# Performance work log

Hardware: AMD Instinct MI355X
Metric: run time of the kernel (lower is better)

Reference implementation:

```python
import jax, jax.numpy as jnp
import numpy as np

T, B, I, H = 512, 64, 1024, 1024
DROPOUT = 0.3


def setup_inputs() -> dict:
    key = jax.random.key(0)
    k = jax.random.split(key, 6)
    s = 1.0 / np.sqrt(H).astype(np.float32)
    x = jax.random.normal(k[0], (T, B, I), dtype=jnp.float32)
    w_ih = jax.random.uniform(k[1], (4 * H, I), minval=-s, maxval=s, dtype=jnp.float32)
    w_hh = jax.random.uniform(k[2], (4 * H, H), minval=-s, maxval=s, dtype=jnp.float32)
    b_ih = jax.random.uniform(k[3], (4 * H,), minval=-s, maxval=s, dtype=jnp.float32)
    b_hh = jax.random.uniform(k[4], (4 * H,), minval=-s, maxval=s, dtype=jnp.float32)
    # init_weights: forget-gate bias (second quarter) set to 1
    b_ih = b_ih.at[H:2 * H].set(1.0)
    b_hh = b_hh.at[H:2 * H].set(1.0)
    # DropConnect mask on recurrent weights (training-mode dropout, fixed realization)
    keep = jax.random.bernoulli(k[5], 1.0 - DROPOUT, (4 * H, H))
    hh_mask = keep.astype(jnp.float32) / (1.0 - DROPOUT)
    return {"x": x, "w_ih": w_ih, "w_hh": w_hh, "b_ih": b_ih, "b_hh": b_hh, "hh_mask": hh_mask}


def reference(x, w_ih, w_hh, b_ih, b_hh, hh_mask):
    # x: (T, B, I). PyTorch LSTM gate order: i, f, g, o.
    h = w_hh.shape[1]
    w_hh_dropped = w_hh * hh_mask  # DropConnect applied once per forward
    # Precompute input contribution for all timesteps (one big GEMM): (T, B, 4H)
    gx = jnp.einsum('tbi,gi->tbg', x, w_ih) + b_ih + b_hh

    def step(carry, g_t):
        h_t, c_t = carry
        gates = g_t + h_t @ w_hh_dropped.T  # (B, 4H)
        i_g, f_g, g_g, o_g = jnp.split(gates, 4, axis=-1)
        i_g = jax.nn.sigmoid(i_g)
        f_g = jax.nn.sigmoid(f_g)
        g_g = jnp.tanh(g_g)
        o_g = jax.nn.sigmoid(o_g)
        c_new = f_g * c_t + i_g * g_g
        h_new = o_g * jnp.tanh(c_new)
        return (h_new, c_new), h_new

    bsz = x.shape[1]
    init = (jnp.zeros((bsz, h), x.dtype), jnp.zeros((bsz, h), x.dtype))
    (hn, cn), out = jax.lax.scan(step, init, gx)
    # match torch: output (T,B,H), hn/cn with leading num_layers dim
    return out, hn[None], cn[None]
```

## Files before the change

### kernel.cpp

```cpp
#include <hip/hip_runtime.h>

#define TT 512
#define BB 64
#define II 1024
#define HH 1024
#define GG 4096
#define BH 65536
#define NBLK 128

typedef __attribute__((ext_vector_type(8))) short bf16x8;
typedef __attribute__((ext_vector_type(4))) float f32x4;
typedef __attribute__((ext_vector_type(4))) unsigned u32x4;

__device__ __forceinline__ float bf2f(unsigned short u) {
  union { unsigned int i; float f; } v; v.i = ((unsigned int)u) << 16; return v.f;
}
__device__ __forceinline__ unsigned short f2bf(float f) {
  union { float f; unsigned int i; } v; v.f = f;
  return (unsigned short)((v.i + 0x7FFFu + ((v.i >> 16) & 1u)) >> 16);
}
__device__ __forceinline__ bf16x8 pack8(float4 a, float4 b) {
  union { bf16x8 v; unsigned short u[8]; } p;
  p.u[0] = f2bf(a.x); p.u[1] = f2bf(a.y); p.u[2] = f2bf(a.z); p.u[3] = f2bf(a.w);
  p.u[4] = f2bf(b.x); p.u[5] = f2bf(b.y); p.u[6] = f2bf(b.z); p.u[7] = f2bf(b.w);
  return p.v;
}
__device__ __forceinline__ float sigmoid_f(float x) { return 1.0f / (1.0f + __expf(-x)); }
__device__ __forceinline__ float tanh_f(float x) {
  float e = __expf(-2.0f * fabsf(x));
  float t = (1.0f - e) / (1.0f + e);
  return copysignf(t, x);
}

__device__ __forceinline__ void st32_uc(unsigned* p, unsigned v) {
  __hip_atomic_store(p, v, __ATOMIC_RELAXED, __HIP_MEMORY_SCOPE_AGENT);
}
__device__ __forceinline__ unsigned ld32_uc(const unsigned* p) {
  return __hip_atomic_load(p, __ATOMIC_RELAXED, __HIP_MEMORY_SCOPE_AGENT);
}
__device__ __forceinline__ void st128_uc(void* p, u32x4 v) {
  asm volatile("global_store_dwordx4 %0, %1, off sc0 sc1" :: "v"(p), "v"(v) : "memory");
}
__device__ __forceinline__ void lds_add_rel(int* p) {
  __hip_atomic_fetch_add(p, 1, __ATOMIC_RELEASE, __HIP_MEMORY_SCOPE_WORKGROUP);
}
__device__ __forceinline__ int lds_ld_acq(const int* p) {
  return __hip_atomic_load(p, __ATOMIC_ACQUIRE, __HIP_MEMORY_SCOPE_WORKGROUP);
}
__device__ __forceinline__ void lds_st_rel(int* p, int v) {
  __hip_atomic_store(p, v, __ATOMIC_RELEASE, __HIP_MEMORY_SCOPE_WORKGROUP);
}

__global__ __launch_bounds__(256) void wdlstm_xconv(
    const float* __restrict__ xc, unsigned short* __restrict__ xbf, int n4) {
  int stride = gridDim.x * blockDim.x;
  for (int i = blockIdx.x * blockDim.x + threadIdx.x; i < n4; i += stride) {
    float4 v = *(const float4*)(xc + (size_t)i * 4);
    unsigned short o[4] = {f2bf(v.x), f2bf(v.y), f2bf(v.z), f2bf(v.w)};
    *(unsigned long long*)(xbf + (size_t)i * 4) = *(unsigned long long*)o;
  }
}

__global__ __launch_bounds__(576) void wdlstm_fused(
    const float* __restrict__ w_hh, const float* __restrict__ hh_mask,
    const float* __restrict__ w_ih,
    const float* __restrict__ b_ih, const float* __restrict__ b_hh,
    const unsigned short* __restrict__ xbf,
    float* __restrict__ out, float* __restrict__ c_state,
    unsigned* __restrict__ flags,
    unsigned short* __restrict__ hinit,
    unsigned short* __restrict__ hring,
    int t0, int tc) {
  __shared__ __align__(16) char Wh[65536];
  __shared__ __align__(16) char Wi[65536];
  __shared__ float Dlds[64][33];
  __shared__ __align__(8) unsigned short Dgx[4][32][72];
  __shared__ __align__(16) unsigned Hs[64][4];
  __shared__ int syncv[8];

  const int tid = threadIdx.x;
  const int wv  = tid >> 6, l = tid & 63;
  const int ln  = l & 15, lq = l >> 4;
  const int j0h = blockIdx.x * 8;
  unsigned* g_prog = flags + 2048;

  for (int c = tid; c < 4096; c += 576) {
    int n = c >> 7, cc = c & 127;
    int wrow = (n >> 3) * HH + j0h + (n & 7);
    int addr = (n * 2048 + cc * 16) ^ ((n & 7) << 4);
    {
      const float* sw = w_hh   + (size_t)wrow * HH + cc * 8;
      const float* sm = hh_mask + (size_t)wrow * HH + cc * 8;
      float4 w0 = *(const float4*)sw, w1 = *(const float4*)(sw + 4);
      float4 m0 = *(const float4*)sm, m1 = *(const float4*)(sm + 4);
      float4 p0 = {w0.x * m0.x, w0.y * m0.y, w0.z * m0.z, w0.w * m0.w};
      float4 p1 = {w1.x * m1.x, w1.y * m1.y, w1.z * m1.z, w1.w * m1.w};
      *(bf16x8*)(Wh + addr) = pack8(p0, p1);
    }
    {
      const float* si = w_ih + (size_t)wrow * II + cc * 8;
      float4 a0 = *(const float4*)si, a1 = *(const float4*)(si + 4);
      *(bf16x8*)(Wi + addr) = pack8(a0, a1);
    }
  }
  if (tid < 8) syncv[tid] = 0;
  __syncthreads();

  if (wv < 4) {
    const int b_ep = l;
    const int jj0  = 2 * wv;
    float c_reg[2];
    if (t0 == 0) { c_reg[0] = c_reg[1] = 0.f; }
    else {
      float2 cv = *(const float2*)(c_state + (size_t)b_ep * HH + j0h + jj0);
      c_reg[0] = cv.x; c_reg[1] = cv.y;
    }
    float biasv[4][2];
#pragma unroll
    for (int g = 0; g < 4; ++g)
#pragma unroll
      for (int q = 0; q < 2; ++q) {
        int col = g * HH + j0h + jj0 + q;
        biasv[g][q] = b_ih[col] + b_hh[col];
      }
    float* hn_out = out + (size_t)TT * BH;
    float* cn_out = hn_out + BH;

    for (int lt = 0; lt < tc; ++lt) {
      const int t = t0 + lt;
      f32x4 acc[2];
      acc[0] = (f32x4){0.f, 0.f, 0.f, 0.f};
      acc[1] = (f32x4){0.f, 0.f, 0.f, 0.f};

      if (t > 0) {
        const unsigned short* hp = (lt == 0) ? hinit : hring + (size_t)(lt - 1) * BH;
        const unsigned short* ap = hp + (size_t)(16 * wv + ln) * HH + lq * 8;
        int avail = (lt == 0) ? 8 : 0;
        auto ensure = [&](int g) {
          while (avail <= g) {
            int v = (int)ld32_uc(g_prog) - 8 * t;
            if (v > 8) v = 8;
            if (v > avail) avail = v; else __builtin_amdgcn_s_sleep(1);
          }
        };
        bf16x8 a0[4], a1[4];
        ensure(0);
#pragma unroll
        for (int i = 0; i < 4; ++i) a0[i] = *(const bf16x8*)(ap + i * 32);
#pragma unroll
        for (int g = 0; g < 8; ++g) {
          bf16x8* cur = (g & 1) ? a1 : a0;
          bf16x8* nxt = (g & 1) ? a0 : a1;
          if (g < 7) {
            ensure(g + 1);
#pragma unroll
            for (int i = 0; i < 4; ++i)
              nxt[i] = *(const bf16x8*)(ap + (4 * (g + 1) + i) * 32);
          }
#pragma unroll
          for (int i = 0; i < 4; ++i) {
            int kc = 4 * g + i;
#pragma unroll
            for (int ni = 0; ni < 2; ++ni) {
              int n = 16 * ni + ln;
              int baddr = (n * 2048 + kc * 64 + lq * 16) ^ ((n & 7) << 4);
              bf16x8 b = *(const bf16x8*)(Wh + baddr);
              acc[ni] = __builtin_amdgcn_mfma_f32_16x16x32_bf16(cur[i], b, acc[ni], 0, 0, 0);
            }
          }
        }
      }
#pragma unroll
      for (int ni = 0; ni < 2; ++ni)
#pragma unroll
        for (int r = 0; r < 4; ++r)
          Dlds[16 * wv + 4 * lq + r][16 * ni + ln] = acc[ni][r];
      if (l == 0) lds_add_rel(&syncv[0]);
      {
        const int tgt = 4 * (lt + 1);
        while (lds_ld_acq(&syncv[0]) < tgt) __builtin_amdgcn_s_sleep(1);
        while (lds_ld_acq(&syncv[2]) < lt + 1 || lds_ld_acq(&syncv[3]) < lt + 1 ||
               lds_ld_acq(&syncv[4]) < lt + 1 || lds_ld_acq(&syncv[5]) < lt + 1)
          __builtin_amdgcn_s_sleep(1);
      }

      const int slot = lt & 3;
      float hq[2];
#pragma unroll
      for (int q = 0; q < 2; ++q) {
        int jj = jj0 + q;
        float g0 = Dlds[b_ep][ 0 + jj] + bf2f(Dgx[slot][ 0 + jj][b_ep]) + biasv[0][q];
        float g1 = Dlds[b_ep][ 8 + jj] + bf2f(Dgx[slot][ 8 + jj][b_ep]) + biasv[1][q];
        float g2 = Dlds[b_ep][16 + jj] + bf2f(Dgx[slot][16 + jj][b_ep]) + biasv[2][q];
        float g3 = Dlds[b_ep][24 + jj] + bf2f(Dgx[slot][24 + jj][b_ep]) + biasv[3][q];
        float ig = sigmoid_f(g0);
        float fg = sigmoid_f(g1);
        float gg = tanh_f(g2);
        float og = sigmoid_f(g3);
        c_reg[q] = fg * c_reg[q] + ig * gg;
        hq[q] = og * tanh_f(c_reg[q]);
      }
      *(float2*)(out + (size_t)t * BH + (size_t)b_ep * HH + j0h + jj0) = make_float2(hq[0], hq[1]);
      Hs[b_ep][wv] = (unsigned)f2bf(hq[0]) | ((unsigned)f2bf(hq[1]) << 16);
      if (t == TT - 1) {
        *(float2*)(hn_out + (size_t)b_ep * HH + j0h + jj0) = make_float2(hq[0], hq[1]);
        *(float2*)(cn_out + (size_t)b_ep * HH + j0h + jj0) = make_float2(c_reg[0], c_reg[1]);
      }
      if (l == 0) lds_add_rel(&syncv[1]);

      if (wv == 0) {
        const int tgt = 4 * (lt + 1);
        while (lds_ld_acq(&syncv[1]) < tgt) __builtin_amdgcn_s_sleep(1);
        u32x4 hv4 = *(const u32x4*)&Hs[l][0];
        char* dst = (char*)hring + ((size_t)lt * BH + (size_t)l * HH + j0h) * 2;
        st128_uc(dst, hv4);
        if (lt == tc - 1) {
          char* dsti = (char*)hinit + ((size_t)l * HH + j0h) * 2;
          st128_uc(dsti, hv4);
        }
        asm volatile("s_waitcnt vmcnt(0)" ::: "memory");
        if (l == 0) st32_uc(&flags[blockIdx.x * 16], (unsigned)(t + 1));
      }
    }
    *(float2*)(c_state + (size_t)b_ep * HH + j0h + jj0) = make_float2(c_reg[0], c_reg[1]);

  } else if (wv < 8) {
    const int w2 = wv - 4;
    for (int s = 0; s < tc; ++s) {
      if (s >= 4) {
        const int tgt = 4 * (s - 3);
        while (lds_ld_acq(&syncv[1]) < tgt) __builtin_amdgcn_s_sleep(1);
      }
      f32x4 acc[2];
      acc[0] = (f32x4){0.f, 0.f, 0.f, 0.f};
      acc[1] = (f32x4){0.f, 0.f, 0.f, 0.f};
      const unsigned short* ap = xbf + (size_t)s * BH + (size_t)(16 * w2 + ln) * II + lq * 8;
      bf16x8 aA[8], aB[8];
#pragma unroll
      for (int i = 0; i < 8; ++i) aA[i] = *(const bf16x8*)(ap + i * 32);
#pragma unroll
      for (int c4 = 0; c4 < 4; ++c4) {
        const bf16x8* cur = (c4 & 1) ? aB : aA;
        bf16x8*       nxt = (c4 & 1) ? aA : aB;
        if (c4 < 3) {
#pragma unroll
          for (int i = 0; i < 8; ++i) nxt[i] = *(const bf16x8*)(ap + (c4 + 1) * 256 + i * 32);
        }
#pragma unroll
        for (int i = 0; i < 8; ++i) {
          int kc = c4 * 8 + i;
#pragma unroll
          for (int ni = 0; ni < 2; ++ni) {
            int n = 16 * ni + ln;
            int baddr = (n * 2048 + kc * 64 + lq * 16) ^ ((n & 7) << 4);
            bf16x8 b = *(const bf16x8*)(Wi + baddr);
            acc[ni] = __builtin_amdgcn_mfma_f32_16x16x32_bf16(cur[i], b, acc[ni], 0, 0, 0);
          }
        }
      }
      const int slot = s & 3;
#pragma unroll
      for (int ni = 0; ni < 2; ++ni) {
        unsigned short p[4] = {f2bf(acc[ni][0]), f2bf(acc[ni][1]),
                               f2bf(acc[ni][2]), f2bf(acc[ni][3])};
        *(unsigned long long*)&Dgx[slot][16 * ni + ln][16 * w2 + 4 * lq] =
            *(unsigned long long*)p;
      }
      if (l == 0) lds_st_rel(&syncv[2 + w2], s + 1);
    }

  } else if (blockIdx.x == 0) {
    const unsigned* f0 = flags + (2 * l) * 16;
    const unsigned* f1 = flags + (2 * l + 1) * 16;
    for (int s = t0 + 1; s < t0 + tc; ++s) {
      int pub = 0;
      while (pub < 8) {
        bool mine = ((int)ld32_uc(f0) >= s) && ((int)ld32_uc(f1) >= s);
        unsigned long long b = __ballot(mine);
        int ng = 0;
        while (ng < 8 && ((b >> (8 * ng)) & 0xFFull) == 0xFFull) ++ng;
        if (ng > pub) {
          pub = ng;
          if (l == 0) st32_uc(g_prog, (unsigned)(8 * s + ng));
        } else {
          __builtin_amdgcn_s_sleep(1);
        }
      }
    }
  }
}

extern "C" void kernel_launch(void* const* d_in, const int* in_sizes, int n_in,
                              void* d_out, int out_size, void* d_ws, size_t ws_size,
                              hipStream_t stream) {
  const float* x       = (const float*)d_in[0];
  const float* w_ih    = (const float*)d_in[1];
  const float* w_hh    = (const float*)d_in[2];
  const float* b_ih    = (const float*)d_in[3];
  const float* b_hh    = (const float*)d_in[4];
  const float* hh_mask = (const float*)d_in[5];
  float* out           = (float*)d_out;

  char* ws = (char*)d_ws;
  float* c_state        = (float*)ws;
  unsigned* flags       = (unsigned*)(ws + 262144);
  unsigned short* hinit = (unsigned short*)(ws + 278528);
  unsigned short* hring = (unsigned short*)(ws + 409600);

  const long long fixed = 409600;
  const long long per_t = 131072 + 131072;
  long long avail = (long long)ws_size - fixed;
  int TC = (int)(avail / per_t);
  if (TC > 128) TC = 128;
  if (TC < 2) TC = 2;
  unsigned short* xbf = (unsigned short*)(ws + 409600 + (size_t)TC * 131072);

  hipMemsetAsync(flags, 0, 16384, stream);

  for (int t0 = 0; t0 < TT; t0 += TC) {
    int tc = TT - t0 < TC ? TT - t0 : TC;
    const float* xc = x + (size_t)t0 * BB * II;
    wdlstm_xconv<<<256, 256, 0, stream>>>(xc, xbf, tc * BH / 4);
    wdlstm_fused<<<NBLK, 576, 0, stream>>>(w_hh, hh_mask, w_ih, b_ih, b_hh, xbf,
                                           out, c_state, flags, hinit, hring, t0, tc);
  }
}
```

Measured before the change: 4.518 ms.

## Fuse x fp32-to-bf16 conversion into LSTM kernel and enlarge time chunks

Removes the separate x conversion kernel: the input-projection waves now load fp32 x directly with nontemporal loads and pack it to bf16 in registers. Because the bf16 x buffer is gone, the workspace holds only the h ring, so the time chunk can grow up to the full sequence, reducing the number of kernel launches and weight reloads. It also raises the wave priority of the elementwise/recurrent waves. The cost is twice the global read traffic for x inside the fused kernel and extra conversion ALU work on the input-projection waves.

Result: slower. 8.330 ms (+84.4%).

```diff
diff --git a/kernel.cpp b/kernel.cpp
--- a/kernel.cpp
+++ b/kernel.cpp
@@ -25,6 +25,12 @@
   p.u[4] = f2bf(b.x); p.u[5] = f2bf(b.y); p.u[6] = f2bf(b.z); p.u[7] = f2bf(b.w);
   return p.v;
 }
+__device__ __forceinline__ bf16x8 pack8v(f32x4 a, f32x4 b) {
+  union { bf16x8 v; unsigned short u[8]; } p;
+  p.u[0] = f2bf(a[0]); p.u[1] = f2bf(a[1]); p.u[2] = f2bf(a[2]); p.u[3] = f2bf(a[3]);
+  p.u[4] = f2bf(b[0]); p.u[5] = f2bf(b[1]); p.u[6] = f2bf(b[2]); p.u[7] = f2bf(b[3]);
+  return p.v;
+}
 __device__ __forceinline__ float sigmoid_f(float x) { return 1.0f / (1.0f + __expf(-x)); }
 __device__ __forceinline__ float tanh_f(float x) {
   float e = __expf(-2.0f * fabsf(x));
@@ -51,21 +57,11 @@
   __hip_atomic_store(p, v, __ATOMIC_RELEASE, __HIP_MEMORY_SCOPE_WORKGROUP);
 }
 
-__global__ __launch_bounds__(256) void wdlstm_xconv(
-    const float* __restrict__ xc, unsigned short* __restrict__ xbf, int n4) {
-  int stride = gridDim.x * blockDim.x;
-  for (int i = blockIdx.x * blockDim.x + threadIdx.x; i < n4; i += stride) {
-    float4 v = *(const float4*)(xc + (size_t)i * 4);
-    unsigned short o[4] = {f2bf(v.x), f2bf(v.y), f2bf(v.z), f2bf(v.w)};
-    *(unsigned long long*)(xbf + (size_t)i * 4) = *(unsigned long long*)o;
-  }
-}
-
 __global__ __launch_bounds__(576) void wdlstm_fused(
     const float* __restrict__ w_hh, const float* __restrict__ hh_mask,
     const float* __restrict__ w_ih,
     const float* __restrict__ b_ih, const float* __restrict__ b_hh,
-    const unsigned short* __restrict__ xbf,
+    const float* __restrict__ x,
     float* __restrict__ out, float* __restrict__ c_state,
     unsigned* __restrict__ flags,
     unsigned short* __restrict__ hinit,
@@ -107,12 +103,13 @@
   __syncthreads();
 
   if (wv < 4) {
-    const int b_ep = l;
+    __builtin_amdgcn_s_setprio(1);
+    const int b_ew = l;
     const int jj0  = 2 * wv;
     float c_reg[2];
     if (t0 == 0) { c_reg[0] = c_reg[1] = 0.f; }
     else {
-      float2 cv = *(const float2*)(c_state + (size_t)b_ep * HH + j0h + jj0);
+      float2 cv = *(const float2*)(c_state + (size_t)b_ew * HH + j0h + jj0);
       c_reg[0] = cv.x; c_reg[1] = cv.y;
     }
     float biasv[4][2];
@@ -189,10 +186,10 @@
 #pragma unroll
       for (int q = 0; q < 2; ++q) {
         int jj = jj0 + q;
-        float g0 = Dlds[b_ep][ 0 + jj] + bf2f(Dgx[slot][ 0 + jj][b_ep]) + biasv[0][q];
-        float g1 = Dlds[b_ep][ 8 + jj] + bf2f(Dgx[slot][ 8 + jj][b_ep]) + biasv[1][q];
-        float g2 = Dlds[b_ep][16 + jj] + bf2f(Dgx[slot][16 + jj][b_ep]) + biasv[2][q];
-        float g3 = Dlds[b_ep][24 + jj] + bf2f(Dgx[slot][24 + jj][b_ep]) + biasv[3][q];
+        float g0 = Dlds[b_ew][ 0 + jj] + bf2f(Dgx[slot][ 0 + jj][b_ew]) + biasv[0][q];
+        float g1 = Dlds[b_ew][ 8 + jj] + bf2f(Dgx[slot][ 8 + jj][b_ew]) + biasv[1][q];
+        float g2 = Dlds[b_ew][16 + jj] + bf2f(Dgx[slot][16 + jj][b_ew]) + biasv[2][q];
+        float g3 = Dlds[b_ew][24 + jj] + bf2f(Dgx[slot][24 + jj][b_ew]) + biasv[3][q];
         float ig = sigmoid_f(g0);
         float fg = sigmoid_f(g1);
         float gg = tanh_f(g2);
@@ -200,11 +197,11 @@
         c_reg[q] = fg * c_reg[q] + ig * gg;
         hq[q] = og * tanh_f(c_reg[q]);
       }
-      *(float2*)(out + (size_t)t * BH + (size_t)b_ep * HH + j0h + jj0) = make_float2(hq[0], hq[1]);
-      Hs[b_ep][wv] = (unsigned)f2bf(hq[0]) | ((unsigned)f2bf(hq[1]) << 16);
+      *(float2*)(out + (size_t)t * BH + (size_t)b_ew * HH + j0h + jj0) = make_float2(hq[0], hq[1]);
+      Hs[b_ew][wv] = (unsigned)f2bf(hq[0]) | ((unsigned)f2bf(hq[1]) << 16);
       if (t == TT - 1) {
-        *(float2*)(hn_out + (size_t)b_ep * HH + j0h + jj0) = make_float2(hq[0], hq[1]);
-        *(float2*)(cn_out + (size_t)b_ep * HH + j0h + jj0) = make_float2(c_reg[0], c_reg[1]);
+        *(float2*)(hn_out + (size_t)b_ew * HH + j0h + jj0) = make_float2(hq[0], hq[1]);
+        *(float2*)(cn_out + (size_t)b_ew * HH + j0h + jj0) = make_float2(c_reg[0], c_reg[1]);
       }
       if (l == 0) lds_add_rel(&syncv[1]);
 
@@ -214,15 +211,13 @@
         u32x4 hv4 = *(const u32x4*)&Hs[l][0];
         char* dst = (char*)hring + ((size_t)lt * BH + (size_t)l * HH + j0h) * 2;
         st128_uc(dst, hv4);
-        if (lt == tc - 1) {
-          char* dsti = (char*)hinit + ((size_t)l * HH + j0h) * 2;
-          st128_uc(dsti, hv4);
-        }
+        if (lt == tc - 1)
+          *(u32x4*)((char*)hinit + ((size_t)l * HH + j0h) * 2) = hv4;
         asm volatile("s_waitcnt vmcnt(0)" ::: "memory");
         if (l == 0) st32_uc(&flags[blockIdx.x * 16], (unsigned)(t + 1));
       }
     }
-    *(float2*)(c_state + (size_t)b_ep * HH + j0h + jj0) = make_float2(c_reg[0], c_reg[1]);
+    *(float2*)(c_state + (size_t)b_ew * HH + j0h + jj0) = make_float2(c_reg[0], c_reg[1]);
 
   } else if (wv < 8) {
     const int w2 = wv - 4;
@@ -234,17 +229,25 @@
       f32x4 acc[2];
       acc[0] = (f32x4){0.f, 0.f, 0.f, 0.f};
       acc[1] = (f32x4){0.f, 0.f, 0.f, 0.f};
-      const unsigned short* ap = xbf + (size_t)s * BH + (size_t)(16 * w2 + ln) * II + lq * 8;
+      const float* ap = x + (size_t)(t0 + s) * BH + (size_t)(16 * w2 + ln) * II + lq * 8;
       bf16x8 aA[8], aB[8];
 #pragma unroll
-      for (int i = 0; i < 8; ++i) aA[i] = *(const bf16x8*)(ap + i * 32);
+      for (int i = 0; i < 8; ++i) {
+        f32x4 u0 = __builtin_nontemporal_load((const f32x4*)(ap + i * 32));
+        f32x4 u1 = __builtin_nontemporal_load((const f32x4*)(ap + i * 32 + 4));
+        aA[i] = pack8v(u0, u1);
+      }
 #pragma unroll
       for (int c4 = 0; c4 < 4; ++c4) {
         const bf16x8* cur = (c4 & 1) ? aB : aA;
         bf16x8*       nxt = (c4 & 1) ? aA : aB;
         if (c4 < 3) {
 #pragma unroll
-          for (int i = 0; i < 8; ++i) nxt[i] = *(const bf16x8*)(ap + (c4 + 1) * 256 + i * 32);
+          for (int i = 0; i < 8; ++i) {
+            f32x4 u0 = __builtin_nontemporal_load((const f32x4*)(ap + (c4 + 1) * 256 + i * 32));
+            f32x4 u1 = __builtin_nontemporal_load((const f32x4*)(ap + (c4 + 1) * 256 + i * 32 + 4));
+            nxt[i] = pack8v(u0, u1);
+          }
         }
 #pragma unroll
         for (int i = 0; i < 8; ++i) {
@@ -308,20 +311,17 @@
   unsigned short* hring = (unsigned short*)(ws + 409600);
 
   const long long fixed = 409600;
-  const long long per_t = 131072 + 131072;
+  const long long per_t = 131072;
   long long avail = (long long)ws_size - fixed;
   int TC = (int)(avail / per_t);
-  if (TC > 128) TC = 128;
+  if (TC > TT) TC = TT;
   if (TC < 2) TC = 2;
-  unsigned short* xbf = (unsigned short*)(ws + 409600 + (size_t)TC * 131072);
-
-  hipMemsetAsync(flags, 0, 16384, stream);
+
+  (void)hipMemsetAsync(flags, 0, 16384, stream);
 
   for (int t0 = 0; t0 < TT; t0 += TC) {
     int tc = TT - t0 < TC ? TT - t0 : TC;
-    const float* xc = x + (size_t)t0 * BB * II;
-    wdlstm_xconv<<<256, 256, 0, stream>>>(xc, xbf, tc * BH / 4);
-    wdlstm_fused<<<NBLK, 576, 0, stream>>>(w_hh, hh_mask, w_ih, b_ih, b_hh, xbf,
+    wdlstm_fused<<<NBLK, 576, 0, stream>>>(w_hh, hh_mask, w_ih, b_ih, b_hh, x,
                                            out, c_state, flags, hinit, hring, t0, tc);
   }
 }
```
